# Optimization experiments

Hardware: AMD Instinct MI355X
Metric: run time of the kernel (lower is better)

## Reference

```python
import jax, jax.numpy as jnp
import numpy as np

B, S, D, NH, FF = 2, 2048, 1024, 16, 4096
HD = D // NH
SCALE = HD ** -0.5
EPS = 1e-5


def layer_norm(x, g, b):
    mu = jnp.mean(x, axis=-1, keepdims=True)
    var = jnp.var(x, axis=-1, keepdims=True)
    return (x - mu) * jax.lax.rsqrt(var + EPS) * g + b


def setup_inputs() -> dict:
    key = jax.random.key(0)
    ks = jax.random.split(key, 12)
    w = 0.02
    return {
        "x": jax.random.normal(ks[0], (B, S, D), dtype=jnp.float32),
        "ln1_g": jnp.ones((D,), jnp.float32),
        "ln1_b": jnp.zeros((D,), jnp.float32),
        "wq": jax.random.normal(ks[1], (D, D), jnp.float32) * w,
        "wkv": jax.random.normal(ks[2], (D, 2 * D), jnp.float32) * w,
        "wo": jax.random.normal(ks[3], (D, D), jnp.float32) * w,
        "bo": jnp.zeros((D,), jnp.float32),
        "ln2_g": jnp.ones((D,), jnp.float32),
        "ln2_b": jnp.zeros((D,), jnp.float32),
        "w1": jax.random.normal(ks[4], (D, FF), jnp.float32) * w,
        "b1": jnp.zeros((FF,), jnp.float32),
        "w2": jax.random.normal(ks[5], (FF, D), jnp.float32) * w,
        "b2": jnp.zeros((D,), jnp.float32),
    }


def reference(x, ln1_g, ln1_b, wq, wkv, wo, bo, ln2_g, ln2_b, w1, b1, w2, b2):
    # pre-norm self-attention (y=None -> keys = normalized queries), no mask
    h = layer_norm(x, ln1_g, ln1_b)                      # [B,S,D]
    q = (h @ wq).reshape(B, S, NH, HD)                   # [B,S,H,hd]
    kv = (h @ wkv).reshape(B, S, 2, NH, HD)
    k, v = kv[:, :, 0], kv[:, :, 1]                      # [B,S,H,hd]
    scores = jnp.einsum("bnhd,bmhd->bnmh", q, k) * SCALE  # [B,S,S,H]
    attn = jax.nn.softmax(scores, axis=2)
    o = jnp.einsum("bnmh,bmhd->bnhd", attn, v).reshape(B, S, D)
    o = o @ wo + bo
    x = x + o
    h2 = layer_norm(x, ln2_g, ln2_b)
    ff = jnp.maximum(h2 @ w1 + b1, 0.0) @ w2 + b2        # relu MLP, dropout p=0
    return (x + ff, attn)
```

## Files before the change

kernel.cpp:

```cpp
#include <hip/hip_runtime.h>
#include <hip/hip_bf16.h>


constexpr int Bc = 2, Sc = 2048, Dc = 1024, NHc = 16, FFc = 4096;
constexpr int Mrows = Bc * Sc;
constexpr float SCALE_ = 0.125f;
constexpr float EPSc = 1e-5f;
constexpr float L2E = 1.4426950408889634f;
constexpr float SC_L2E = SCALE_ * L2E;

typedef __attribute__((ext_vector_type(8))) short short8;
typedef __attribute__((ext_vector_type(4))) short short4v;
typedef __attribute__((ext_vector_type(4))) float floatx4;

#define DEV static __device__ __forceinline__

DEV short f2b(float f) {
  union { float f; unsigned u; } v; v.f = f;
  unsigned r = v.u + 0x7FFFu + ((v.u >> 16) & 1u);
  return (short)(r >> 16);
}

DEV floatx4 mfma16(short8 a, short8 b, floatx4 c) {
  return __builtin_amdgcn_mfma_f32_16x16x32_bf16(a, b, c, 0, 0, 0);
}

__global__ __launch_bounds__(256) void cast_transpose_k(
    const float* __restrict__ W, short* __restrict__ Wt, int K, int N) {
  __shared__ float t[32][33];
  int n0 = blockIdx.x * 32, k0 = blockIdx.y * 32;
  int tx = threadIdx.x & 31, ty = threadIdx.x >> 5;
  for (int r = ty; r < 32; r += 8)
    t[r][tx] = W[(size_t)(k0 + r) * N + n0 + tx];
  __syncthreads();
  for (int r = ty; r < 32; r += 8)
    Wt[(size_t)(n0 + r) * K + k0 + tx] = f2b(t[tx][r]);
}

__global__ __launch_bounds__(256) void layernorm_k(
    const float* __restrict__ x, const float* __restrict__ g,
    const float* __restrict__ bb, short* __restrict__ out) {
  int row = blockIdx.x;
  float4 v = ((const float4*)(x + (size_t)row * Dc))[threadIdx.x];
  float s = v.x + v.y + v.z + v.w;
  float s2 = v.x * v.x + v.y * v.y + v.z * v.z + v.w * v.w;
#pragma unroll
  for (int off = 32; off >= 1; off >>= 1) {
    s += __shfl_xor(s, off);
    s2 += __shfl_xor(s2, off);
  }
  __shared__ float red[8];
  int wave = threadIdx.x >> 6, lane = threadIdx.x & 63;
  if (lane == 0) { red[wave] = s; red[4 + wave] = s2; }
  __syncthreads();
  s = red[0] + red[1] + red[2] + red[3];
  s2 = red[4] + red[5] + red[6] + red[7];
  float mu = s * (1.0f / Dc);
  float var = s2 * (1.0f / Dc) - mu * mu;
  float rstd = rsqrtf(var + EPSc);
  int c = threadIdx.x * 4;
  float4 gv = ((const float4*)g)[threadIdx.x];
  float4 bv = ((const float4*)bb)[threadIdx.x];
  short4v o;
  o.x = f2b((v.x - mu) * rstd * gv.x + bv.x);
  o.y = f2b((v.y - mu) * rstd * gv.y + bv.y);
  o.z = f2b((v.z - mu) * rstd * gv.z + bv.z);
  o.w = f2b((v.w - mu) * rstd * gv.w + bv.w);
  *(short4v*)(out + (size_t)row * Dc + c) = o;
}

template <int OUTF>
__global__ __launch_bounds__(256) void gemm_bt_k(
    const short* __restrict__ A, const short* __restrict__ Bt,
    const float* __restrict__ bias, const float* __restrict__ resid,
    void* __restrict__ Cout, int M, int N, int K, int relu) {
  constexpr int PAD = 40;
  __shared__ short As[128 * PAD];
  __shared__ short Bs[128 * PAD];
  int tid = threadIdx.x;
  int wave = tid >> 6, lane = tid & 63, quad = lane >> 4, l16 = lane & 15;
  int m0 = blockIdx.y * 128, n0 = blockIdx.x * 128;
  int wm = (wave & 1) * 64, wn = (wave >> 1) * 64;
  int srow = tid >> 1, scol = (tid & 1) * 16;
  floatx4 acc[4][4] = {};
  for (int k0 = 0; k0 < K; k0 += 32) {
    const short8* ap = (const short8*)(A + (size_t)(m0 + srow) * K + k0 + scol);
    short8 a0 = ap[0], a1 = ap[1];
    const short8* bp = (const short8*)(Bt + (size_t)(n0 + srow) * K + k0 + scol);
    short8 b0 = bp[0], b1 = bp[1];
    __syncthreads();
    *(short8*)(&As[srow * PAD + scol]) = a0;
    *(short8*)(&As[srow * PAD + scol + 8]) = a1;
    *(short8*)(&Bs[srow * PAD + scol]) = b0;
    *(short8*)(&Bs[srow * PAD + scol + 8]) = b1;
    __syncthreads();
    short8 af[4], bf[4];
#pragma unroll
    for (int i = 0; i < 4; ++i)
      af[i] = *(const short8*)(&As[(wm + i * 16 + l16) * PAD + quad * 8]);
#pragma unroll
    for (int j = 0; j < 4; ++j)
      bf[j] = *(const short8*)(&Bs[(wn + j * 16 + l16) * PAD + quad * 8]);
#pragma unroll
    for (int i = 0; i < 4; ++i)
#pragma unroll
      for (int j = 0; j < 4; ++j)
        acc[i][j] = mfma16(af[i], bf[j], acc[i][j]);
  }
#pragma unroll
  for (int i = 0; i < 4; ++i) {
    int row = m0 + wm + i * 16 + quad * 4;
#pragma unroll
    for (int j = 0; j < 4; ++j) {
      int col = n0 + wn + j * 16 + l16;
      float bv = bias ? bias[col] : 0.0f;
#pragma unroll
      for (int r = 0; r < 4; ++r) {
        float v = acc[i][j][r] + bv;
        if (resid) v += resid[(size_t)(row + r) * N + col];
        if (relu) v = fmaxf(v, 0.0f);
        if (OUTF == 0)
          ((short*)Cout)[(size_t)(row + r) * N + col] = f2b(v);
        else
          ((float*)Cout)[(size_t)(row + r) * N + col] = v;
      }
    }
  }
}

__global__ __launch_bounds__(256) void transpose_v_k(
    const short* __restrict__ kv, short* __restrict__ vT) {
  __shared__ short t[64][65];
  int bh = blockIdx.y, b = bh >> 4, h = bh & 15;
  int m0 = blockIdx.x * 64;
  int c = threadIdx.x & 63, ty = threadIdx.x >> 6;
  for (int r = ty; r < 64; r += 4)
    t[r][c] = kv[(size_t)(b * Sc + m0 + r) * 2048 + 1024 + h * 64 + c];
  __syncthreads();
  for (int dd = ty; dd < 64; dd += 4)
    vT[((size_t)bh * 64 + dd) * Sc + m0 + c] = t[c][dd];
}

__global__ __launch_bounds__(256) void attn_stats_k(
    const short* __restrict__ q, const short* __restrict__ kv,
    float* __restrict__ m_i, float* __restrict__ inv_l) {
  int bh = blockIdx.y, b = bh >> 4, h = bh & 15;
  int wave = threadIdx.x >> 6, lane = threadIdx.x & 63, quad = lane >> 4,
      l16 = lane & 15;
  int n0 = blockIdx.x * 64 + wave * 16;
  const short* qp = q + (size_t)(b * Sc + n0 + l16) * Dc + h * 64 + quad * 8;
  short8 qf0 = *(const short8*)qp;
  short8 qf1 = *(const short8*)(qp + 32);
  const short* kb = kv + (size_t)b * Sc * 2048 + h * 64 + quad * 8;
  float rm[4], rl[4];
#pragma unroll
  for (int r = 0; r < 4; ++r) { rm[r] = -1e30f; rl[r] = 0.0f; }
  for (int m0 = 0; m0 < Sc; m0 += 16) {
    const short* kp = kb + (size_t)(m0 + l16) * 2048;
    short8 kf0 = *(const short8*)kp;
    short8 kf1 = *(const short8*)(kp + 32);
    floatx4 s = {0.0f, 0.0f, 0.0f, 0.0f};
    s = mfma16(qf0, kf0, s);
    s = mfma16(qf1, kf1, s);
#pragma unroll
    for (int r = 0; r < 4; ++r) {
      float sv = s[r] * SC_L2E;
      if (sv <= rm[r]) {
        rl[r] += exp2f(sv - rm[r]);
      } else {
        rl[r] = rl[r] * exp2f(rm[r] - sv) + 1.0f;
        rm[r] = sv;
      }
    }
  }
#pragma unroll
  for (int off = 1; off < 16; off <<= 1) {
#pragma unroll
    for (int r = 0; r < 4; ++r) {
      float om = __shfl_xor(rm[r], off);
      float ol = __shfl_xor(rl[r], off);
      float nm = fmaxf(rm[r], om);
      rl[r] = rl[r] * exp2f(rm[r] - nm) + ol * exp2f(om - nm);
      rm[r] = nm;
    }
  }
  if (l16 == 0) {
    int n = n0 + quad * 4;
#pragma unroll
    for (int r = 0; r < 4; ++r) {
      m_i[(size_t)bh * Sc + n + r] = rm[r];
      inv_l[(size_t)bh * Sc + n + r] = 1.0f / rl[r];
    }
  }
}

__global__ __launch_bounds__(256) void attn_write_k(
    const short* __restrict__ q, const short* __restrict__ kv,
    const float* __restrict__ m_i, const float* __restrict__ inv_l,
    float* __restrict__ attn) {
  constexpr int HP = 17;
  __shared__ float P[32 * 16 * HP];
  __shared__ float sm[16][32], sl[16][32];
  int b = blockIdx.z;
  int n0 = blockIdx.y * 32, m0 = blockIdx.x * 16;
  int tid = threadIdx.x;
  int wave = tid >> 6, lane = tid & 63, quad = lane >> 4, l16 = lane & 15;
  for (int i = tid; i < 512; i += 256) {
    int h = i >> 5, nn = i & 31;
    sm[h][nn] = m_i[(size_t)(b * 16 + h) * Sc + n0 + nn];
    sl[h][nn] = inv_l[(size_t)(b * 16 + h) * Sc + n0 + nn];
  }
  __syncthreads();
#pragma unroll
  for (int hh = 0; hh < 4; ++hh) {
    int h = wave * 4 + hh;
    const short* kp = kv + (size_t)(b * Sc + m0 + l16) * 2048 + h * 64 + quad * 8;
    short8 kf0 = *(const short8*)kp;
    short8 kf1 = *(const short8*)(kp + 32);
#pragma unroll
    for (int ni = 0; ni < 2; ++ni) {
      const short* qp =
          q + (size_t)(b * Sc + n0 + ni * 16 + l16) * Dc + h * 64 + quad * 8;
      short8 qf0 = *(const short8*)qp;
      short8 qf1 = *(const short8*)(qp + 32);
      floatx4 s = {0.0f, 0.0f, 0.0f, 0.0f};
      s = mfma16(qf0, kf0, s);
      s = mfma16(qf1, kf1, s);
#pragma unroll
      for (int r = 0; r < 4; ++r) {
        int nn = ni * 16 + quad * 4 + r;
        float p = exp2f(s[r] * SC_L2E - sm[h][nn]) * sl[h][nn];
        P[(nn * 16 + l16) * HP + h] = p;
      }
    }
  }
  __syncthreads();
  size_t base = ((size_t)(b * Sc + n0) * Sc + m0) * 16;
  int m = tid >> 4, h = tid & 15;
  for (int n = 0; n < 32; ++n)
    attn[base + (size_t)n * (Sc * 16) + m * 16 + h] = P[(n * 16 + m) * HP + h];
}

__global__ __launch_bounds__(256) void attn_pv_k(
    const short* __restrict__ q, const short* __restrict__ kv,
    const short* __restrict__ vT, const float* __restrict__ m_i,
    const float* __restrict__ inv_l, short* __restrict__ o) {
  constexpr int PPAD = 40;
  __shared__ short P[4][16 * PPAD];
  int bh = blockIdx.y, b = bh >> 4, h = bh & 15;
  int wave = threadIdx.x >> 6, lane = threadIdx.x & 63, quad = lane >> 4,
      l16 = lane & 15;
  int n0 = blockIdx.x * 64 + wave * 16;
  const short* qp = q + (size_t)(b * Sc + n0 + l16) * Dc + h * 64 + quad * 8;
  short8 qf0 = *(const short8*)qp;
  short8 qf1 = *(const short8*)(qp + 32);
  float mm[4], il[4];
#pragma unroll
  for (int r = 0; r < 4; ++r) {
    int n = n0 + quad * 4 + r;
    mm[r] = m_i[(size_t)bh * Sc + n];
    il[r] = inv_l[(size_t)bh * Sc + n];
  }
  floatx4 oacc[4] = {};
  const short* kb = kv + (size_t)b * Sc * 2048 + h * 64 + quad * 8;
  const short* vb = vT + (size_t)bh * 64 * Sc;
  short* myP = &P[wave][0];
  for (int m0 = 0; m0 < Sc; m0 += 32) {
#pragma unroll
    for (int ms = 0; ms < 2; ++ms) {
      const short* kp = kb + (size_t)(m0 + ms * 16 + l16) * 2048;
      short8 kf0 = *(const short8*)kp;
      short8 kf1 = *(const short8*)(kp + 32);
      floatx4 s = {0.0f, 0.0f, 0.0f, 0.0f};
      s = mfma16(qf0, kf0, s);
      s = mfma16(qf1, kf1, s);
#pragma unroll
      for (int r = 0; r < 4; ++r) {
        float p = exp2f(s[r] * SC_L2E - mm[r]);
        myP[(quad * 4 + r) * PPAD + ms * 16 + l16] = f2b(p);
      }
    }
    short8 pf = *(const short8*)(&myP[l16 * PPAD + quad * 8]);
#pragma unroll
    for (int ds = 0; ds < 4; ++ds) {
      short8 vf = *(const short8*)(vb + (size_t)(ds * 16 + l16) * Sc + m0 + quad * 8);
      oacc[ds] = mfma16(pf, vf, oacc[ds]);
    }
  }
#pragma unroll
  for (int ds = 0; ds < 4; ++ds)
#pragma unroll
    for (int r = 0; r < 4; ++r)
      o[(size_t)(b * Sc + n0 + quad * 4 + r) * Dc + h * 64 + ds * 16 + l16] =
          f2b(oacc[ds][r] * il[r]);
}

extern "C" void kernel_launch(void* const* d_in, const int* in_sizes, int n_in,
                              void* d_out, int out_size, void* d_ws,
                              size_t ws_size, hipStream_t stream) {
  const float* x = (const float*)d_in[0];
  const float* ln1g = (const float*)d_in[1];
  const float* ln1b = (const float*)d_in[2];
  const float* wq = (const float*)d_in[3];
  const float* wkv = (const float*)d_in[4];
  const float* wo = (const float*)d_in[5];
  const float* bo = (const float*)d_in[6];
  const float* ln2g = (const float*)d_in[7];
  const float* ln2b = (const float*)d_in[8];
  const float* w1 = (const float*)d_in[9];
  const float* b1 = (const float*)d_in[10];
  const float* w2 = (const float*)d_in[11];
  const float* b2 = (const float*)d_in[12];

  char* ws = (char*)d_ws;
  const size_t MB = 1024 * 1024;
  short* wqT  = (short*)(ws + 0 * MB);
  short* wkvT = (short*)(ws + 2 * MB);
  short* woT  = (short*)(ws + 6 * MB);
  short* w1T  = (short*)(ws + 8 * MB);
  short* w2T  = (short*)(ws + 16 * MB);
  short* h    = (short*)(ws + 24 * MB);
  float* x2   = (float*)(ws + 32 * MB);
  float* m_i  = (float*)(ws + 48 * MB);
  float* invl = (float*)(ws + 48 * MB + 256 * 1024);
  short* o    = (short*)(ws + 49 * MB);
  short* qb   = (short*)(ws + 57 * MB);
  short* kvb  = (short*)(ws + 65 * MB);
  short* vT   = (short*)(ws + 81 * MB);
  short* ff1  = (short*)(ws + 57 * MB);

  float* out0 = (float*)d_out;
  float* attn = (float*)d_out + (size_t)Bc * Sc * Dc;

  cast_transpose_k<<<dim3(Dc / 32, Dc / 32), 256, 0, stream>>>(wq, wqT, Dc, Dc);
  cast_transpose_k<<<dim3(2048 / 32, Dc / 32), 256, 0, stream>>>(wkv, wkvT, Dc, 2048);
  cast_transpose_k<<<dim3(Dc / 32, Dc / 32), 256, 0, stream>>>(wo, woT, Dc, Dc);
  cast_transpose_k<<<dim3(FFc / 32, Dc / 32), 256, 0, stream>>>(w1, w1T, Dc, FFc);
  cast_transpose_k<<<dim3(Dc / 32, FFc / 32), 256, 0, stream>>>(w2, w2T, FFc, Dc);

  layernorm_k<<<Mrows, 256, 0, stream>>>(x, ln1g, ln1b, h);

  gemm_bt_k<0><<<dim3(Dc / 128, Mrows / 128), 256, 0, stream>>>(
      h, wqT, nullptr, nullptr, qb, Mrows, Dc, Dc, 0);
  gemm_bt_k<0><<<dim3(2048 / 128, Mrows / 128), 256, 0, stream>>>(
      h, wkvT, nullptr, nullptr, kvb, Mrows, 2048, Dc, 0);

  transpose_v_k<<<dim3(Sc / 64, Bc * NHc), 256, 0, stream>>>(kvb, vT);
  attn_stats_k<<<dim3(Sc / 64, Bc * NHc), 256, 0, stream>>>(qb, kvb, m_i, invl);
  attn_write_k<<<dim3(Sc / 16, Sc / 32, Bc), 256, 0, stream>>>(qb, kvb, m_i, invl, attn);
  attn_pv_k<<<dim3(Sc / 64, Bc * NHc), 256, 0, stream>>>(qb, kvb, vT, m_i, invl, o);

  gemm_bt_k<1><<<dim3(Dc / 128, Mrows / 128), 256, 0, stream>>>(
      o, woT, bo, x, x2, Mrows, Dc, Dc, 0);
  layernorm_k<<<Mrows, 256, 0, stream>>>(x2, ln2g, ln2b, h);
  gemm_bt_k<0><<<dim3(FFc / 128, Mrows / 128), 256, 0, stream>>>(
      h, w1T, b1, nullptr, ff1, Mrows, FFc, Dc, 1);
  gemm_bt_k<1><<<dim3(Dc / 128, Mrows / 128), 256, 0, stream>>>(
      ff1, w2T, b2, x2, out0, Mrows, Dc, FFc, 0);
}
```

Measured before the change: 1.428 ms.

## Use direct global-to-LDS loads in GEMM and vectorize attention probability writes

The GEMM staging now uses global_load_lds to move A and B tiles straight into unpadded shared memory instead of going through registers, which cuts register traffic and VGPR use. Each wave loads two 16-row slabs of the tile. Separately, the attention-probability write kernel pads its shared buffer to 20 floats per row and stores float4 vectors to the large attn output, replacing scalar stores. Dropping the LDS padding can bring back bank conflicts on the MFMA fragment reads.

```diff
diff --git a/kernel.cpp b/kernel.cpp
--- a/kernel.cpp
+++ b/kernel.cpp
@@ -23,6 +23,12 @@
 
 DEV floatx4 mfma16(short8 a, short8 b, floatx4 c) {
   return __builtin_amdgcn_mfma_f32_16x16x32_bf16(a, b, c, 0, 0, 0);
+}
+
+DEV void load_lds16(const short* g, short* l) {
+  __builtin_amdgcn_global_load_lds(
+      (const __attribute__((address_space(1))) void*)g,
+      (__attribute__((address_space(3))) void*)l, 16, 0, 0);
 }
 
 __global__ __launch_bounds__(256) void cast_transpose_k(
@@ -74,33 +80,36 @@
     const short* __restrict__ A, const short* __restrict__ Bt,
     const float* __restrict__ bias, const float* __restrict__ resid,
     void* __restrict__ Cout, int M, int N, int K, int relu) {
-  constexpr int PAD = 40;
-  __shared__ short As[128 * PAD];
-  __shared__ short Bs[128 * PAD];
+  __shared__ short As[128 * 32];
+  __shared__ short Bs[128 * 32];
   int tid = threadIdx.x;
   int wave = tid >> 6, lane = tid & 63, quad = lane >> 4, l16 = lane & 15;
   int m0 = blockIdx.y * 128, n0 = blockIdx.x * 128;
   int wm = (wave & 1) * 64, wn = (wave >> 1) * 64;
-  int srow = tid >> 1, scol = (tid & 1) * 16;
+  int lrow = lane >> 2, lcol = (lane & 3) * 8;
+  const short* Ab0 = A + (size_t)(m0 + wave * 32 + lrow) * K + lcol;
+  const short* Ab1 = A + (size_t)(m0 + wave * 32 + 16 + lrow) * K + lcol;
+  const short* Bb0 = Bt + (size_t)(n0 + wave * 32 + lrow) * K + lcol;
+  const short* Bb1 = Bt + (size_t)(n0 + wave * 32 + 16 + lrow) * K + lcol;
+  short* Al0 = &As[(wave * 2 + 0) * 512];
+  short* Al1 = &As[(wave * 2 + 1) * 512];
+  short* Bl0 = &Bs[(wave * 2 + 0) * 512];
+  short* Bl1 = &Bs[(wave * 2 + 1) * 512];
   floatx4 acc[4][4] = {};
   for (int k0 = 0; k0 < K; k0 += 32) {
-    const short8* ap = (const short8*)(A + (size_t)(m0 + srow) * K + k0 + scol);
-    short8 a0 = ap[0], a1 = ap[1];
-    const short8* bp = (const short8*)(Bt + (size_t)(n0 + srow) * K + k0 + scol);
-    short8 b0 = bp[0], b1 = bp[1];
     __syncthreads();
-    *(short8*)(&As[srow * PAD + scol]) = a0;
-    *(short8*)(&As[srow * PAD + scol + 8]) = a1;
-    *(short8*)(&Bs[srow * PAD + scol]) = b0;
-    *(short8*)(&Bs[srow * PAD + scol + 8]) = b1;
+    load_lds16(Ab0 + k0, Al0);
+    load_lds16(Ab1 + k0, Al1);
+    load_lds16(Bb0 + k0, Bl0);
+    load_lds16(Bb1 + k0, Bl1);
     __syncthreads();
     short8 af[4], bf[4];
 #pragma unroll
     for (int i = 0; i < 4; ++i)
-      af[i] = *(const short8*)(&As[(wm + i * 16 + l16) * PAD + quad * 8]);
+      af[i] = *(const short8*)(&As[(wm + i * 16 + l16) * 32 + quad * 8]);
 #pragma unroll
     for (int j = 0; j < 4; ++j)
-      bf[j] = *(const short8*)(&Bs[(wn + j * 16 + l16) * PAD + quad * 8]);
+      bf[j] = *(const short8*)(&Bs[(wn + j * 16 + l16) * 32 + quad * 8]);
 #pragma unroll
     for (int i = 0; i < 4; ++i)
 #pragma unroll
@@ -198,7 +207,7 @@
     const short* __restrict__ q, const short* __restrict__ kv,
     const float* __restrict__ m_i, const float* __restrict__ inv_l,
     float* __restrict__ attn) {
-  constexpr int HP = 17;
+  constexpr int HP = 20;
   __shared__ float P[32 * 16 * HP];
   __shared__ float sm[16][32], sl[16][32];
   int b = blockIdx.z;
@@ -236,9 +245,12 @@
   }
   __syncthreads();
   size_t base = ((size_t)(b * Sc + n0) * Sc + m0) * 16;
-  int m = tid >> 4, h = tid & 15;
-  for (int n = 0; n < 32; ++n)
-    attn[base + (size_t)n * (Sc * 16) + m * 16 + h] = P[(n * 16 + m) * HP + h];
+  int w = tid >> 6, l = tid & 63;
+  int ml = l >> 2, h4 = (l & 3) * 4;
+  for (int n = w; n < 32; n += 4) {
+    float4 v = *(const float4*)&P[(n * 16 + ml) * HP + h4];
+    *(float4*)&attn[base + (size_t)n * (Sc * 16) + ml * 16 + h4] = v;
+  }
 }
 
 __global__ __launch_bounds__(256) void attn_pv_k(
```

Measured after the change: 1.425 ms. About the same (-0.3%).
